# Kernel optimization log

Measured on AMD Instinct MI355X. Metric: run time of the kernel, lower is better.

## Reference

```python
import jax, jax.numpy as jnp
import numpy as np

N = 33554432          # flat genome length (multiple of chunk_size -> no padding)
CS = 64               # chunk_size
REF = 16              # ref_dim
HID = 64              # hidden
SPLIT = N // 2        # weight_coords[0]: policy/meta split index


def setup_inputs() -> dict:
    key = jax.random.key(0)
    ks = jax.random.split(key, 12)
    nc = N // CS
    rn = lambda k, shape, sc=1.0: jax.random.normal(k, shape, dtype=jnp.float32) * sc
    return {
        "flat_weights": rn(ks[0], (N,)),
        "other_weights": rn(ks[1], (N,)),
        "weight_coords": jnp.array([SPLIT], dtype=jnp.int32),
        "noise": rn(ks[2], (nc, CS)),                      # unit gaussian, scaled inside
        "w_enc": rn(ks[3], (REF, CS), 0.1),
        "b_enc": jnp.zeros((REF,), jnp.float32),
        "w_c1": rn(ks[4], (HID, 3 * REF), 0.1),
        "b_c1": jnp.zeros((HID,), jnp.float32),
        "w_c2": rn(ks[5], (CS, HID), 0.1),
        "b_c2": jnp.zeros((CS,), jnp.float32),
        "w_g1": rn(ks[6], (HID, 4 * REF), 0.1),
        "b_g1": jnp.zeros((HID,), jnp.float32),
        "w_g2": rn(ks[7], (2, HID), 0.1),
        "b_g2": jnp.zeros((2,), jnp.float32),
        "ref_policy": rn(ks[8], (REF,), 0.1),
        "ref_meta": rn(ks[9], (REF,), 0.1),
        "cs_policy": jnp.array(0.03, jnp.float32),
        "cs_meta": jnp.array(0.01, jnp.float32),
        "es_policy": jnp.array(0.01, jnp.float32),
        "es_meta": jnp.array(0.002, jnp.float32),
    }


def _encode(x, w_enc, b_enc):
    # nn.Sequential(Linear(CS->REF), Tanh())
    return jnp.tanh(x @ w_enc.T + b_enc)


def reference(flat_weights, other_weights, weight_coords, noise,
              w_enc, b_enc, w_c1, b_c1, w_c2, b_c2,
              w_g1, b_g1, w_g2, b_g2,
              ref_policy, ref_meta, cs_policy, cs_meta, es_policy, es_meta):
    split = weight_coords[0]
    a = flat_weights.reshape(-1, CS)     # [nc, CS]
    b = other_weights.reshape(-1, CS)    # [nc, CS]

    # ---- gated crossover blend (sigmoid mode, clamp = 0) ----
    ea = _encode(a, w_enc, b_enc)
    eb = _encode(b, w_enc, b_enc)
    gate_in = jnp.concatenate([ea, eb, ea - eb, ea * eb], axis=1)  # [nc, 4*REF]
    logits = jnp.tanh(gate_in @ w_g1.T + b_g1) @ w_g2.T + b_g2     # [nc, 2]
    alpha = jax.nn.sigmoid(logits[:, 0] - logits[:, 1])[:, None]   # [nc, 1]
    base = alpha * a + (1.0 - alpha) * b

    # ---- dual-head (policy/meta) masked correction ----
    nc = base.shape[0]
    mask = (jnp.arange(nc, dtype=jnp.int32) * CS < split)[:, None]  # True -> policy
    enc = _encode(base, w_enc, b_enc)                               # [nc, REF]
    ref = jnp.where(mask, ref_policy, ref_meta)                     # [nc, REF]
    x = jnp.concatenate([enc, ref, enc - ref], axis=1)              # [nc, 3*REF]
    corr = jnp.tanh(jnp.tanh(x @ w_c1.T + b_c1) @ w_c2.T + b_c2)    # [nc, CS]
    corr = jnp.clip(corr * jnp.where(mask, cs_policy, cs_meta), -0.1, 0.1)

    # ---- masked exploration noise ----
    mutated = base + corr + noise * jnp.where(mask, es_policy, es_meta)
    return mutated.reshape(-1)[:N]
```

## Files before the change

### kernel.cpp

```cpp
#include <hip/hip_runtime.h>
#include <math.h>

#define NTOT 33554432
#define CS 64
#define REF 16
#define HID 64
#define NC (NTOT / CS)

#define WS_FLOATS 8320

#if defined(__has_builtin)
#if __has_builtin(__builtin_amdgcn_rcpf)
#define FAST_RCP(x) __builtin_amdgcn_rcpf(x)
#endif
#endif
#ifndef FAST_RCP
#define FAST_RCP(x) (1.0f / (x))
#endif

__device__ __forceinline__ float fast_tanh(float x) {
  float e = __expf(2.0f * x);
  return 1.0f - 2.0f * FAST_RCP(e + 1.0f);
}

__device__ __forceinline__ float get4(const float4& v, int c) {
  return c == 0 ? v.x : c == 1 ? v.y : c == 2 ? v.z : v.w;
}

__global__ void setup_fold_kernel(const float* __restrict__ w_g1,
                                  const float* __restrict__ w_c1,
                                  const float* __restrict__ b_c1,
                                  const float* __restrict__ w_c2,
                                  const float* __restrict__ ref_p,
                                  const float* __restrict__ ref_m,
                                  float* __restrict__ ws) {
  const int t = threadIdx.x;
  for (int idx = t; idx < 1024; idx += 256) {
    const int j = idx >> 4, k = idx & 15;
    ws[idx]        = w_g1[j * 64 + k] + w_g1[j * 64 + 32 + k];
    ws[1024 + idx] = w_g1[j * 64 + 16 + k] - w_g1[j * 64 + 32 + k];
    ws[2048 + idx] = w_g1[j * 64 + 48 + k];
    ws[3072 + idx] = w_c1[j * 48 + k] + w_c1[j * 48 + 32 + k];
  }
  if (t < 64) {
    float sp = b_c1[t], sm = b_c1[t];
    for (int k = 0; k < REF; ++k) {
      const float wd = w_c1[t * 48 + 16 + k] - w_c1[t * 48 + 32 + k];
      sp += ref_p[k] * wd;
      sm += ref_m[k] * wd;
    }
    ws[4096 + t] = sp;
    ws[4160 + t] = sm;
  }
  for (int idx = t; idx < 4096; idx += 256) {
    const int j = idx >> 6, i = idx & 63;
    ws[4224 + idx] = w_c2[i * 64 + j];
  }
}

template <bool USE_WS>
__global__ __launch_bounds__(256) void dual_mutate_kernel(
    const float* __restrict__ A, const float* __restrict__ B,
    const int* __restrict__ coords, const float* __restrict__ noise,
    const float* __restrict__ w_enc, const float* __restrict__ b_enc,
    const float* __restrict__ w_c1, const float* __restrict__ b_c1,
    const float* __restrict__ w_c2, const float* __restrict__ b_c2,
    const float* __restrict__ w_g1, const float* __restrict__ b_g1,
    const float* __restrict__ w_g2, const float* __restrict__ b_g2,
    const float* __restrict__ ref_p, const float* __restrict__ ref_m,
    const float* __restrict__ cs_p, const float* __restrict__ cs_m,
    const float* __restrict__ es_p, const float* __restrict__ es_m,
    const float* __restrict__ ws, float* __restrict__ out) {
  const int chunk = blockIdx.x * blockDim.x + threadIdx.x;
  if (chunk >= NC) return;
  const size_t off = (size_t)chunk * CS;
  const float* ap = A + off;
  const float* bp = B + off;

  float ea[REF], eb[REF];
#pragma unroll
  for (int j = 0; j < REF; ++j) {
    const float bj = b_enc[j];
    ea[j] = bj;
    eb[j] = bj;
  }
#pragma unroll 4
  for (int k4 = 0; k4 < CS / 4; ++k4) {
    const float4 a4 = *reinterpret_cast<const float4*>(ap + 4 * k4);
    const float4 b4 = *reinterpret_cast<const float4*>(bp + 4 * k4);
#pragma unroll
    for (int c = 0; c < 4; ++c) {
      const float av = get4(a4, c);
      const float bv = get4(b4, c);
      const int k = 4 * k4 + c;
#pragma unroll
      for (int j = 0; j < REF; ++j) {
        const float w = w_enc[j * CS + k];
        ea[j] = fmaf(av, w, ea[j]);
        eb[j] = fmaf(bv, w, eb[j]);
      }
    }
  }
#pragma unroll
  for (int j = 0; j < REF; ++j) {
    ea[j] = fast_tanh(ea[j]);
    eb[j] = fast_tanh(eb[j]);
  }

  float pp[REF], dd[REF];
#pragma unroll
  for (int j = 0; j < REF; ++j) {
    pp[j] = ea[j] * eb[j];
    dd[j] = ea[j] - eb[j];
  }
  float l0 = b_g2[0], l1 = b_g2[1];
#pragma unroll 2
  for (int j = 0; j < HID; ++j) {
    float acc = b_g1[j];
    if (USE_WS) {
#pragma unroll
      for (int k = 0; k < REF; ++k) {
        acc = fmaf(ea[k], ws[j * REF + k], acc);
        acc = fmaf(eb[k], ws[1024 + j * REF + k], acc);
        acc = fmaf(pp[k], ws[2048 + j * REF + k], acc);
      }
    } else {
#pragma unroll
      for (int k = 0; k < REF; ++k) {
        acc = fmaf(ea[k], w_g1[j * 64 + k], acc);
        acc = fmaf(eb[k], w_g1[j * 64 + 16 + k], acc);
        acc = fmaf(dd[k], w_g1[j * 64 + 32 + k], acc);
        acc = fmaf(pp[k], w_g1[j * 64 + 48 + k], acc);
      }
    }
    const float h = fast_tanh(acc);
    l0 = fmaf(w_g2[j], h, l0);
    l1 = fmaf(w_g2[HID + j], h, l1);
  }
  const float alpha = FAST_RCP(1.0f + __expf(l1 - l0));

  const int split = coords[0];
  const bool policy = (chunk * CS) < split;

  float base[CS];
  float enc[REF];
#pragma unroll
  for (int j = 0; j < REF; ++j) enc[j] = b_enc[j];
#pragma unroll
  for (int k4 = 0; k4 < CS / 4; ++k4) {
    const float4 a4 = *reinterpret_cast<const float4*>(ap + 4 * k4);
    const float4 b4 = *reinterpret_cast<const float4*>(bp + 4 * k4);
#pragma unroll
    for (int c = 0; c < 4; ++c) {
      const int k = 4 * k4 + c;
      const float av = get4(a4, c);
      const float bv = get4(b4, c);
      const float bb = fmaf(alpha, av - bv, bv);
      base[k] = bb;
#pragma unroll
      for (int j = 0; j < REF; ++j) enc[j] = fmaf(bb, w_enc[j * CS + k], enc[j]);
    }
  }
#pragma unroll
  for (int j = 0; j < REF; ++j) enc[j] = fast_tanh(enc[j]);

  float corr[CS];
#pragma unroll
  for (int i = 0; i < CS; ++i) corr[i] = b_c2[i];

  float rr[REF];
  if (!USE_WS) {
#pragma unroll
    for (int k = 0; k < REF; ++k) rr[k] = policy ? ref_p[k] : ref_m[k];
  }

#pragma unroll 1
  for (int j = 0; j < HID; ++j) {
    float acc;
    if (USE_WS) {
      acc = policy ? ws[4096 + j] : ws[4160 + j];
#pragma unroll
      for (int k = 0; k < REF; ++k) acc = fmaf(enc[k], ws[3072 + j * REF + k], acc);
    } else {
      acc = b_c1[j];
#pragma unroll
      for (int k = 0; k < REF; ++k) {
        acc = fmaf(enc[k], w_c1[j * 48 + k], acc);
        acc = fmaf(rr[k], w_c1[j * 48 + 16 + k], acc);
        acc = fmaf(enc[k] - rr[k], w_c1[j * 48 + 32 + k], acc);
      }
    }
    const float h = fast_tanh(acc);
#pragma unroll
    for (int i = 0; i < CS; ++i) {
      const float w = USE_WS ? ws[4224 + j * 64 + i] : w_c2[i * 64 + j];
      corr[i] = fmaf(w, h, corr[i]);
    }
  }

  const float csv = policy ? cs_p[0] : cs_m[0];
  const float esv = policy ? es_p[0] : es_m[0];
  const float* np_ = noise + off;
  float* op = out + off;
#pragma unroll
  for (int k4 = 0; k4 < CS / 4; ++k4) {
    const float4 n4 = *reinterpret_cast<const float4*>(np_ + 4 * k4);
    float4 o;
#pragma unroll
    for (int c = 0; c < 4; ++c) {
      const int k = 4 * k4 + c;
      float cv = fast_tanh(corr[k]) * csv;
      cv = fminf(fmaxf(cv, -0.1f), 0.1f);
      const float v = base[k] + cv + get4(n4, c) * esv;
      if (c == 0) o.x = v;
      else if (c == 1) o.y = v;
      else if (c == 2) o.z = v;
      else o.w = v;
    }
    *reinterpret_cast<float4*>(op + 4 * k4) = o;
  }
}

extern "C" void kernel_launch(void* const* d_in, const int* in_sizes, int n_in,
                              void* d_out, int out_size, void* d_ws, size_t ws_size,
                              hipStream_t stream) {
  const float* A     = (const float*)d_in[0];
  const float* B     = (const float*)d_in[1];
  const int*   coord = (const int*)d_in[2];
  const float* noise = (const float*)d_in[3];
  const float* w_enc = (const float*)d_in[4];
  const float* b_enc = (const float*)d_in[5];
  const float* w_c1  = (const float*)d_in[6];
  const float* b_c1  = (const float*)d_in[7];
  const float* w_c2  = (const float*)d_in[8];
  const float* b_c2  = (const float*)d_in[9];
  const float* w_g1  = (const float*)d_in[10];
  const float* b_g1  = (const float*)d_in[11];
  const float* w_g2  = (const float*)d_in[12];
  const float* b_g2  = (const float*)d_in[13];
  const float* ref_p = (const float*)d_in[14];
  const float* ref_m = (const float*)d_in[15];
  const float* cs_p  = (const float*)d_in[16];
  const float* cs_m  = (const float*)d_in[17];
  const float* es_p  = (const float*)d_in[18];
  const float* es_m  = (const float*)d_in[19];
  float* out = (float*)d_out;
  float* ws  = (float*)d_ws;

  const bool use_ws = ws_size >= WS_FLOATS * sizeof(float);
  const int blocks = NC / 256;

  if (use_ws) {
    setup_fold_kernel<<<1, 256, 0, stream>>>(w_g1, w_c1, b_c1, w_c2, ref_p, ref_m, ws);
    dual_mutate_kernel<true><<<blocks, 256, 0, stream>>>(
        A, B, coord, noise, w_enc, b_enc, w_c1, b_c1, w_c2, b_c2, w_g1, b_g1,
        w_g2, b_g2, ref_p, ref_m, cs_p, cs_m, es_p, es_m, ws, out);
  } else {
    dual_mutate_kernel<false><<<blocks, 256, 0, stream>>>(
        A, B, coord, noise, w_enc, b_enc, w_c1, b_c1, w_c2, b_c2, w_g1, b_g1,
        w_g2, b_g2, ref_p, ref_m, cs_p, cs_m, es_p, es_m, ws, out);
  }
}
```

Before: 407.7 us.

## Exploit encoder linearity and restructure correction MLP to avoid large register arrays

```diff
diff --git a/kernel.cpp b/kernel.cpp
--- a/kernel.cpp
+++ b/kernel.cpp
@@ -7,7 +7,7 @@
 #define HID 64
 #define NC (NTOT / CS)
 
-#define WS_FLOATS 8320
+#define WS_FLOATS 4224
 
 #if defined(__has_builtin)
 #if __has_builtin(__builtin_amdgcn_rcpf)
@@ -30,7 +30,6 @@
 __global__ void setup_fold_kernel(const float* __restrict__ w_g1,
                                   const float* __restrict__ w_c1,
                                   const float* __restrict__ b_c1,
-                                  const float* __restrict__ w_c2,
                                   const float* __restrict__ ref_p,
                                   const float* __restrict__ ref_m,
                                   float* __restrict__ ws) {
@@ -52,22 +51,15 @@
     ws[4096 + t] = sp;
     ws[4160 + t] = sm;
   }
-  for (int idx = t; idx < 4096; idx += 256) {
-    const int j = idx >> 6, i = idx & 63;
-    ws[4224 + idx] = w_c2[i * 64 + j];
-  }
-}
-
-template <bool USE_WS>
+}
+
 __global__ __launch_bounds__(256) void dual_mutate_kernel(
     const float* __restrict__ A, const float* __restrict__ B,
     const int* __restrict__ coords, const float* __restrict__ noise,
     const float* __restrict__ w_enc, const float* __restrict__ b_enc,
-    const float* __restrict__ w_c1, const float* __restrict__ b_c1,
     const float* __restrict__ w_c2, const float* __restrict__ b_c2,
-    const float* __restrict__ w_g1, const float* __restrict__ b_g1,
-    const float* __restrict__ w_g2, const float* __restrict__ b_g2,
-    const float* __restrict__ ref_p, const float* __restrict__ ref_m,
+    const float* __restrict__ b_g1, const float* __restrict__ w_g2,
+    const float* __restrict__ b_g2,
     const float* __restrict__ cs_p, const float* __restrict__ cs_m,
     const float* __restrict__ es_p, const float* __restrict__ es_m,
     const float* __restrict__ ws, float* __restrict__ out) {
@@ -77,14 +69,14 @@
   const float* ap = A + off;
   const float* bp = B + off;
 
-  float ea[REF], eb[REF];
+  float za[REF], zb[REF];
 #pragma unroll
   for (int j = 0; j < REF; ++j) {
     const float bj = b_enc[j];
-    ea[j] = bj;
-    eb[j] = bj;
-  }
-#pragma unroll 4
+    za[j] = bj;
+    zb[j] = bj;
+  }
+#pragma unroll 2
   for (int k4 = 0; k4 < CS / 4; ++k4) {
     const float4 a4 = *reinterpret_cast<const float4*>(ap + 4 * k4);
     const float4 b4 = *reinterpret_cast<const float4*>(bp + 4 * k4);
@@ -96,42 +88,28 @@
 #pragma unroll
       for (int j = 0; j < REF; ++j) {
         const float w = w_enc[j * CS + k];
-        ea[j] = fmaf(av, w, ea[j]);
-        eb[j] = fmaf(bv, w, eb[j]);
+        za[j] = fmaf(av, w, za[j]);
+        zb[j] = fmaf(bv, w, zb[j]);
       }
     }
   }
+
+  float ea[REF], eb[REF], pp[REF];
 #pragma unroll
   for (int j = 0; j < REF; ++j) {
-    ea[j] = fast_tanh(ea[j]);
-    eb[j] = fast_tanh(eb[j]);
-  }
-
-  float pp[REF], dd[REF];
-#pragma unroll
-  for (int j = 0; j < REF; ++j) {
+    ea[j] = fast_tanh(za[j]);
+    eb[j] = fast_tanh(zb[j]);
     pp[j] = ea[j] * eb[j];
-    dd[j] = ea[j] - eb[j];
   }
   float l0 = b_g2[0], l1 = b_g2[1];
 #pragma unroll 2
   for (int j = 0; j < HID; ++j) {
     float acc = b_g1[j];
-    if (USE_WS) {
-#pragma unroll
-      for (int k = 0; k < REF; ++k) {
-        acc = fmaf(ea[k], ws[j * REF + k], acc);
-        acc = fmaf(eb[k], ws[1024 + j * REF + k], acc);
-        acc = fmaf(pp[k], ws[2048 + j * REF + k], acc);
-      }
-    } else {
-#pragma unroll
-      for (int k = 0; k < REF; ++k) {
-        acc = fmaf(ea[k], w_g1[j * 64 + k], acc);
-        acc = fmaf(eb[k], w_g1[j * 64 + 16 + k], acc);
-        acc = fmaf(dd[k], w_g1[j * 64 + 32 + k], acc);
-        acc = fmaf(pp[k], w_g1[j * 64 + 48 + k], acc);
-      }
+#pragma unroll
+    for (int k = 0; k < REF; ++k) {
+      acc = fmaf(ea[k], ws[j * REF + k], acc);
+      acc = fmaf(eb[k], ws[1024 + j * REF + k], acc);
+      acc = fmaf(pp[k], ws[2048 + j * REF + k], acc);
     }
     const float h = fast_tanh(acc);
     l0 = fmaf(w_g2[j], h, l0);
@@ -141,82 +119,48 @@
 
   const int split = coords[0];
   const bool policy = (chunk * CS) < split;
-
-  float base[CS];
   float enc[REF];
 #pragma unroll
-  for (int j = 0; j < REF; ++j) enc[j] = b_enc[j];
-#pragma unroll
-  for (int k4 = 0; k4 < CS / 4; ++k4) {
-    const float4 a4 = *reinterpret_cast<const float4*>(ap + 4 * k4);
-    const float4 b4 = *reinterpret_cast<const float4*>(bp + 4 * k4);
-#pragma unroll
-    for (int c = 0; c < 4; ++c) {
-      const int k = 4 * k4 + c;
-      const float av = get4(a4, c);
-      const float bv = get4(b4, c);
-      const float bb = fmaf(alpha, av - bv, bv);
-      base[k] = bb;
-#pragma unroll
-      for (int j = 0; j < REF; ++j) enc[j] = fmaf(bb, w_enc[j * CS + k], enc[j]);
-    }
-  }
-#pragma unroll
-  for (int j = 0; j < REF; ++j) enc[j] = fast_tanh(enc[j]);
-
-  float corr[CS];
-#pragma unroll
-  for (int i = 0; i < CS; ++i) corr[i] = b_c2[i];
-
-  float rr[REF];
-  if (!USE_WS) {
-#pragma unroll
-    for (int k = 0; k < REF; ++k) rr[k] = policy ? ref_p[k] : ref_m[k];
-  }
-
-#pragma unroll 1
+  for (int j = 0; j < REF; ++j)
+    enc[j] = fast_tanh(fmaf(alpha, za[j] - zb[j], zb[j]));
+
+  float h[HID];
+#pragma unroll
   for (int j = 0; j < HID; ++j) {
-    float acc;
-    if (USE_WS) {
-      acc = policy ? ws[4096 + j] : ws[4160 + j];
-#pragma unroll
-      for (int k = 0; k < REF; ++k) acc = fmaf(enc[k], ws[3072 + j * REF + k], acc);
-    } else {
-      acc = b_c1[j];
-#pragma unroll
-      for (int k = 0; k < REF; ++k) {
-        acc = fmaf(enc[k], w_c1[j * 48 + k], acc);
-        acc = fmaf(rr[k], w_c1[j * 48 + 16 + k], acc);
-        acc = fmaf(enc[k] - rr[k], w_c1[j * 48 + 32 + k], acc);
-      }
-    }
-    const float h = fast_tanh(acc);
-#pragma unroll
-    for (int i = 0; i < CS; ++i) {
-      const float w = USE_WS ? ws[4224 + j * 64 + i] : w_c2[i * 64 + j];
-      corr[i] = fmaf(w, h, corr[i]);
-    }
+    const float c0p = ws[4096 + j];
+    const float c0m = ws[4160 + j];
+    float acc = policy ? c0p : c0m;
+#pragma unroll
+    for (int k = 0; k < REF; ++k) acc = fmaf(enc[k], ws[3072 + j * REF + k], acc);
+    h[j] = fast_tanh(acc);
   }
 
   const float csv = policy ? cs_p[0] : cs_m[0];
   const float esv = policy ? es_p[0] : es_m[0];
   const float* np_ = noise + off;
   float* op = out + off;
-#pragma unroll
+#pragma unroll 1
   for (int k4 = 0; k4 < CS / 4; ++k4) {
+    const float4 a4 = *reinterpret_cast<const float4*>(ap + 4 * k4);
+    const float4 b4 = *reinterpret_cast<const float4*>(bp + 4 * k4);
     const float4 n4 = *reinterpret_cast<const float4*>(np_ + 4 * k4);
+    float vals[4];
+#pragma unroll
+    for (int c = 0; c < 4; ++c) {
+      const int i = 4 * k4 + c;
+      const float av = get4(a4, c);
+      const float bv = get4(b4, c);
+      const float bb = fmaf(alpha, av - bv, bv);
+      float corr = b_c2[i];
+      const float* wrow = w_c2 + (size_t)i * HID;
+#pragma unroll
+      for (int j = 0; j < HID; ++j) corr = fmaf(h[j], wrow[j], corr);
+      float cv = fast_tanh(corr) * csv;
+      cv = fminf(fmaxf(cv, -0.1f), 0.1f);
+      vals[c] = bb + cv + get4(n4, c) * esv;
+    }
     float4 o;
-#pragma unroll
-    for (int c = 0; c < 4; ++c) {
-      const int k = 4 * k4 + c;
-      float cv = fast_tanh(corr[k]) * csv;
-      cv = fminf(fmaxf(cv, -0.1f), 0.1f);
-      const float v = base[k] + cv + get4(n4, c) * esv;
-      if (c == 0) o.x = v;
-      else if (c == 1) o.y = v;
-      else if (c == 2) o.z = v;
-      else o.w = v;
-    }
+    o.x = vals[0]; o.y = vals[1]; o.z = vals[2]; o.w = vals[3];
     *reinterpret_cast<float4*>(op + 4 * k4) = o;
   }
 }
@@ -247,17 +191,10 @@
   float* out = (float*)d_out;
   float* ws  = (float*)d_ws;
 
-  const bool use_ws = ws_size >= WS_FLOATS * sizeof(float);
+  setup_fold_kernel<<<1, 256, 0, stream>>>(w_g1, w_c1, b_c1, ref_p, ref_m, ws);
+
   const int blocks = NC / 256;
-
-  if (use_ws) {
-    setup_fold_kernel<<<1, 256, 0, stream>>>(w_g1, w_c1, b_c1, w_c2, ref_p, ref_m, ws);
-    dual_mutate_kernel<true><<<blocks, 256, 0, stream>>>(
-        A, B, coord, noise, w_enc, b_enc, w_c1, b_c1, w_c2, b_c2, w_g1, b_g1,
-        w_g2, b_g2, ref_p, ref_m, cs_p, cs_m, es_p, es_m, ws, out);
-  } else {
-    dual_mutate_kernel<false><<<blocks, 256, 0, stream>>>(
-        A, B, coord, noise, w_enc, b_enc, w_c1, b_c1, w_c2, b_c2, w_g1, b_g1,
-        w_g2, b_g2, ref_p, ref_m, cs_p, cs_m, es_p, es_m, ws, out);
-  }
-}
+  dual_mutate_kernel<<<blocks, 256, 0, stream>>>(
+      A, B, coord, noise, w_enc, b_enc, w_c2, b_c2, b_g1,
+      w_g2, b_g2, cs_p, cs_m, es_p, es_m, ws, out);
+}
```

After: 700.7 us. +71.8%, slower.
